# Optimization experiments

Hardware: AMD Instinct MI355X
Metric: run time of the kernel (lower is better)

The kernel has to match this reference:

```python
import jax, jax.numpy as jnp
import numpy as np

D_MODEL = 1024
N_HEADS = 16
HEAD_DIM = D_MODEL // N_HEADS
SEQ = 2048
BATCH = 2
ROPE_BASE = 10000.0


def _rope(x, start_pos):
    # x: [B, S, H, hd]; interleaved-pair RoPE (Llama view_as_complex convention)
    S, hd = x.shape[1], x.shape[3]
    inv_freq = 1.0 / (ROPE_BASE ** (jnp.arange(0, hd, 2, dtype=jnp.float32) / hd))
    pos = jnp.arange(start_pos, start_pos + S, dtype=jnp.float32)
    freqs = pos[:, None] * inv_freq[None, :]          # [S, hd/2]
    cos = jnp.cos(freqs)[None, :, None, :]            # [1, S, 1, hd/2]
    sin = jnp.sin(freqs)[None, :, None, :]
    x1 = x[..., 0::2]
    x2 = x[..., 1::2]
    r1 = x1 * cos - x2 * sin
    r2 = x1 * sin + x2 * cos
    return jnp.stack([r1, r2], axis=-1).reshape(x.shape)


def setup_inputs() -> dict:
    key = jax.random.key(0)
    ks = jax.random.split(key, 5)
    scale = 1.0 / np.sqrt(D_MODEL)
    x = jax.random.normal(ks[0], (BATCH, SEQ, D_MODEL), dtype=jnp.float32)
    Wq = jax.random.normal(ks[1], (D_MODEL, D_MODEL), dtype=jnp.float32) * scale
    Wk = jax.random.normal(ks[2], (D_MODEL, D_MODEL), dtype=jnp.float32) * scale
    Wv = jax.random.normal(ks[3], (D_MODEL, D_MODEL), dtype=jnp.float32) * scale
    Wo = jax.random.normal(ks[4], (D_MODEL, D_MODEL), dtype=jnp.float32) * scale
    # causal mask: True = masked (strictly upper triangular)
    mask = jnp.triu(jnp.ones((SEQ, SEQ), dtype=bool), k=1)[None, None, :, :]
    return {"x": x, "mask": mask, "Wq": Wq, "Wk": Wk, "Wv": Wv, "Wo": Wo}


def reference(x, mask, Wq, Wk, Wv, Wo):
    B, S, D = x.shape
    H, hd = N_HEADS, HEAD_DIM
    scale = 1.0 / np.sqrt(hd)
    start_pos = 0  # prefill, no kv_cache

    # torch nn.Linear(bias=False): y = x @ W.T
    q = jnp.einsum('bsd,ed->bse', x, Wq).reshape(B, S, H, hd)
    k = jnp.einsum('bsd,ed->bse', x, Wk).reshape(B, S, H, hd)
    v = jnp.einsum('bsd,ed->bse', x, Wv).reshape(B, S, H, hd)

    q = _rope(q, start_pos)
    k = _rope(k, start_pos)

    q = q.transpose(0, 2, 1, 3)  # [B, H, S, hd]
    k = k.transpose(0, 2, 1, 3)
    v = v.transpose(0, 2, 1, 3)
    new_kv_cache = (k, v)

    scores = jnp.einsum('bhqd,bhkd->bhqk', q, k) * scale   # [B,H,S,S]
    scores = jnp.where(mask, -jnp.inf, scores)
    attn = jax.nn.softmax(scores, axis=-1)                 # dropout is identity (eval)
    out = jnp.einsum('bhqk,bhkd->bhqd', attn, v)
    out = out.transpose(0, 2, 1, 3).reshape(B, S, D)
    out = jnp.einsum('bsd,ed->bse', out, Wo)
    return (out, new_kv_cache)
```

## Files before the change

kernel.cpp:

```cpp
#include <hip/hip_runtime.h>
#include <hip/hip_bf16.h>
#include <stdint.h>

#define D_MODEL 1024
#define SEQ     2048
#define BATCH   2
#define NH      16
#define HD      64
#define MROWS   (BATCH*SEQ)
#define XN      (MROWS*D_MODEL)
#define WN      (D_MODEL*D_MODEL)

typedef __attribute__((ext_vector_type(8))) __bf16 bf16x8;
typedef __attribute__((ext_vector_type(4))) __bf16 bf16x4;
typedef __attribute__((ext_vector_type(4))) float  floatx4;

#define MFMA(a,b,c) __builtin_amdgcn_mfma_f32_16x16x32_bf16((a),(b),(c),0,0,0)

__device__ __forceinline__ void g2l16(const void* g, void* l) {
    __builtin_amdgcn_global_load_lds(
        (const __attribute__((address_space(1))) void*)g,
        (__attribute__((address_space(3))) void*)l, 16, 0, 0);
}

__global__ __launch_bounds__(256) void cvt_kernel(
    const float* __restrict__ x,  const float* __restrict__ wq,
    const float* __restrict__ wk, const float* __restrict__ wv,
    const float* __restrict__ wo, __bf16* __restrict__ ws)
{
    const int y = blockIdx.y;
    const float* src;
    __bf16* dst;
    int n;
    if (y == 0) { src = x; dst = ws; n = XN; }
    else {
        n = WN;
        src = (y == 1) ? wq : (y == 2) ? wk : (y == 3) ? wv : wo;
        dst = ws + XN + (y - 1) * WN;
    }
    const int i = (blockIdx.x * 256 + threadIdx.x) * 4;
    if (i < n) {
        float4 f = *(const float4*)(src + i);
        bf16x4 o;
        o[0] = (__bf16)f.x; o[1] = (__bf16)f.y;
        o[2] = (__bf16)f.z; o[3] = (__bf16)f.w;
        *(bf16x4*)(dst + i) = o;
    }
}

__device__ __forceinline__ void gemm128_core(
    const __bf16* __restrict__ A, const __bf16* __restrict__ W,
    int m0, int n0, __bf16* ldsA, __bf16* ldsB, floatx4 acc[4][4])
{
    const int tid  = threadIdx.x;
    const int w    = tid >> 6;
    const int lane = tid & 63;
    const int quad = lane >> 4;
    const int ln   = lane & 15;
    const int wm   = (w >> 1) << 6;
    const int wn   = (w & 1) << 6;

    const int r0c = tid >> 2, ch = tid & 3;
    const __bf16* gA0 = A + (m0 + r0c) * D_MODEL + ch * 8;
    const __bf16* gA1 = gA0 + 64 * D_MODEL;
    const __bf16* gB0 = W + (n0 + r0c) * D_MODEL + ch * 8;
    const __bf16* gB1 = gB0 + 64 * D_MODEL;
    const int lofs = w * 512;

    g2l16(gA0, ldsA + lofs);
    g2l16(gA1, ldsA + 2048 + lofs);
    g2l16(gB0, ldsB + lofs);
    g2l16(gB1, ldsB + 2048 + lofs);
    __syncthreads();

    for (int k0 = 0; k0 < D_MODEL; k0 += 32) {
        const int cur = (k0 >> 5) & 1;
        const int nxt = cur ^ 1;
        if (k0 + 32 < D_MODEL) {
            g2l16(gA0 + k0 + 32, ldsA + nxt * 4096 + lofs);
            g2l16(gA1 + k0 + 32, ldsA + nxt * 4096 + 2048 + lofs);
            g2l16(gB0 + k0 + 32, ldsB + nxt * 4096 + lofs);
            g2l16(gB1 + k0 + 32, ldsB + nxt * 4096 + 2048 + lofs);
        }
        const __bf16* cA = ldsA + cur * 4096;
        const __bf16* cB = ldsB + cur * 4096;
        bf16x8 af[4], bfr[4];
        #pragma unroll
        for (int mt = 0; mt < 4; ++mt)
            af[mt] = *(const bf16x8*)(cA + (wm + mt * 16 + ln) * 32 + quad * 8);
        #pragma unroll
        for (int nt = 0; nt < 4; ++nt)
            bfr[nt] = *(const bf16x8*)(cB + (wn + nt * 16 + ln) * 32 + quad * 8);
        #pragma unroll
        for (int mt = 0; mt < 4; ++mt)
            #pragma unroll
            for (int nt = 0; nt < 4; ++nt)
                acc[mt][nt] = MFMA(af[mt], bfr[nt], acc[mt][nt]);
        __syncthreads();
    }
}

__global__ __launch_bounds__(256) void qkv_rope_kernel(
    const __bf16* __restrict__ x,  const __bf16* __restrict__ Wq,
    const __bf16* __restrict__ Wk, const __bf16* __restrict__ Wv,
    __bf16* __restrict__ q_ws, __bf16* __restrict__ k_bf,
    __bf16* __restrict__ vT_ws,
    float* __restrict__ k_out, float* __restrict__ v_out)
{
    const int id  = blockIdx.x;
    const int xcd = id & 7;
    const int sl  = id >> 3;
    const int mb  = (xcd & 3) * 8 + (sl & 7);
    const int yz  = (xcd >> 2) * 12 + (sl >> 3);
    const int nb  = yz & 7;
    const int which = yz >> 3;

    const __bf16* W = (which == 0) ? Wq : (which == 1) ? Wk : Wv;
    const int m0 = mb * 128;
    const int n0 = nb * 128;

    __shared__ __align__(16) __bf16 ldsA[2 * 128 * 32];
    __shared__ __align__(16) __bf16 ldsB[2 * 128 * 32];

    floatx4 acc[4][4] = {};
    gemm128_core(x, W, m0, n0, ldsA, ldsB, acc);

    const int lane = threadIdx.x & 63;
    const int w    = threadIdx.x >> 6;
    const int quad = lane >> 4;
    const int ln   = lane & 15;
    const int wm   = m0 + ((w >> 1) << 6);
    const int wn   = n0 + ((w & 1) << 6);

    #pragma unroll
    for (int nt = 0; nt < 4; ++nt) {
        const int e = wn + nt * 16 + ln;
        const int h = e >> 6;
        const int d = e & 63;
        const float invf = (which < 2)
            ? exp2f(-(float)(d & ~1) * 0.20762050593046014f) : 0.f;
        #pragma unroll
        for (int mt = 0; mt < 4; ++mt) {
            floatx4 c = acc[mt][nt];
            const int mbase = wm + mt * 16 + quad * 4;
            if (which < 2) {
                #pragma unroll
                for (int r = 0; r < 4; ++r) {
                    const int s = (mbase + r) & (SEQ - 1);
                    float self  = c[r];
                    float other = __shfl_xor(self, 1);
                    float sn, cs;
                    __sincosf((float)s * invf, &sn, &cs);
                    c[r] = (lane & 1) ? (other * sn + self * cs)
                                      : (self * cs - other * sn);
                }
            }
            const int b = mbase >> 11;
            const int s = mbase & (SEQ - 1);
            const int idx = ((b * NH + h) * SEQ + s) * HD + d;
            #pragma unroll
            for (int r = 0; r < 4; ++r) {
                if (which == 0) {
                    q_ws[idx + r * HD] = (__bf16)c[r];
                } else if (which == 1) {
                    k_out[idx + r * HD] = c[r];
                    k_bf[idx + r * HD]  = (__bf16)c[r];
                } else {
                    v_out[idx + r * HD] = c[r];
                }
            }
            if (which == 2) {
                bf16x4 pk;
                pk[0] = (__bf16)c[0]; pk[1] = (__bf16)c[1];
                pk[2] = (__bf16)c[2]; pk[3] = (__bf16)c[3];
                *(bf16x4*)(vT_ws + ((b * NH + h) * HD + d) * SEQ + s) = pk;
            }
        }
    }
}

__global__ __launch_bounds__(256, 4) void attn_kernel(
    const __bf16* __restrict__ q_ws, const __bf16* __restrict__ k_all,
    const __bf16* __restrict__ vT,   __bf16* __restrict__ attn_ws)
{
    const int id   = blockIdx.x;
    const int xcd  = id & 7;
    const int sl   = id >> 3;
    const int bh   = xcd * 4 + (sl & 3);
    const int qt   = 31 - (sl >> 2);
    const int w    = threadIdx.x >> 6;
    const int lane = threadIdx.x & 63;
    const int quad = lane >> 4;
    const int ln   = lane & 15;
    const int r0   = qt * 64 + w * 16;

    const __bf16* qb = q_ws + bh * SEQ * HD;
    const __bf16* kb = k_all + bh * SEQ * HD;
    const __bf16* vb = vT + bh * HD * SEQ;

    __shared__ __align__(16) __bf16 ldsK[2][64 * 64];
    __shared__ __align__(16) __bf16 ldsV[2][64 * 64];
    __shared__ __align__(16) __bf16 ldsp[4][16 * 64];
    __bf16* lp = &ldsp[w][0];

    const bf16x8 aq0 = *(const bf16x8*)(qb + (r0 + ln) * HD + quad * 8);
    const bf16x8 aq1 = *(const bf16x8*)(qb + (r0 + ln) * HD + 32 + quad * 8);

    const int nk = qt + 1;

    const int r8 = lane >> 3;
    const int cl = (lane & 7) ^ r8;
    const int rA = w * 16 + r8;
    const int rB = rA + 8;

    const int pc0 = ((quad    ) ^ (ln & 7)) << 3;
    const int pc1 = ((quad | 4) ^ (ln & 7)) << 3;

    auto stage = [&](int bsel, int j0) {
        g2l16(kb + (j0 + rA) * HD + cl * 8, &ldsK[bsel][(w * 16)     * 64]);
        g2l16(kb + (j0 + rB) * HD + cl * 8, &ldsK[bsel][(w * 16 + 8) * 64]);
        g2l16(vb + rA * SEQ + j0 + cl * 8,  &ldsV[bsel][(w * 16)     * 64]);
        g2l16(vb + rB * SEQ + j0 + cl * 8,  &ldsV[bsel][(w * 16 + 8) * 64]);
    };

    floatx4 acc[4] = {};
    float l_part[4] = {0.f, 0.f, 0.f, 0.f};

    stage(0, 0);
    __syncthreads();

    for (int tk = 0; tk < nk; ++tk) {
        const int buf = tk & 1;
        if (tk + 1 < nk) stage(buf ^ 1, (tk + 1) << 6);

        const __bf16* Kb = &ldsK[buf][0];
        const __bf16* Vb = &ldsV[buf][0];
        bf16x8 K[8], V[8];
        #pragma unroll
        for (int nt = 0; nt < 4; ++nt) {
            const int rowo = (nt * 16 + ln) * 64;
            K[nt * 2 + 0] = *(const bf16x8*)(Kb + rowo + pc0);
            K[nt * 2 + 1] = *(const bf16x8*)(Kb + rowo + pc1);
            V[nt * 2 + 0] = *(const bf16x8*)(Vb + rowo + pc0);
            V[nt * 2 + 1] = *(const bf16x8*)(Vb + rowo + pc1);
        }

        floatx4 s[4] = {};
        #pragma unroll
        for (int nt = 0; nt < 4; ++nt) {
            s[nt] = MFMA(aq0, K[nt * 2 + 0], s[nt]);
            s[nt] = MFMA(aq1, K[nt * 2 + 1], s[nt]);
        }

        if (tk == nk - 1) {
            const int j0 = tk << 6;
            #pragma unroll
            for (int nt = 0; nt < 4; ++nt) {
                const int col = j0 + nt * 16 + ln;
                #pragma unroll
                for (int r = 0; r < 4; ++r)
                    if (col > r0 + quad * 4 + r) s[nt][r] = -1e30f;
            }
        }

        floatx4 p[4];
        #pragma unroll
        for (int nt = 0; nt < 4; ++nt)
            #pragma unroll
            for (int r = 0; r < 4; ++r)
                p[nt][r] = __expf(fmaf(s[nt][r], 0.125f, -20.f));
        #pragma unroll
        for (int r = 0; r < 4; ++r)
            l_part[r] += (p[0][r] + p[1][r]) + (p[2][r] + p[3][r]);

        #pragma unroll
        for (int nt = 0; nt < 4; ++nt) {
            const int cchunk = nt * 2 + (ln >> 3);
            #pragma unroll
            for (int r = 0; r < 4; ++r) {
                const int row = quad * 4 + r;
                lp[row * 64 + ((cchunk ^ (row & 7)) << 3) + (ln & 7)] =
                    (__bf16)p[nt][r];
            }
        }
        const bf16x8 ap0 = *(const bf16x8*)(lp + ln * 64 + pc0);
        const bf16x8 ap1 = *(const bf16x8*)(lp + ln * 64 + pc1);

        #pragma unroll
        for (int nt = 0; nt < 4; ++nt) {
            acc[nt] = MFMA(ap0, V[nt * 2 + 0], acc[nt]);
            acc[nt] = MFMA(ap1, V[nt * 2 + 1], acc[nt]);
        }
        __syncthreads();
    }

    const int b = bh >> 4, h = bh & 15;
    #pragma unroll
    for (int r = 0; r < 4; ++r) {
        float l = l_part[r];
        l += __shfl_xor(l, 1);
        l += __shfl_xor(l, 2);
        l += __shfl_xor(l, 4);
        l += __shfl_xor(l, 8);
        const float inv = 1.f / fmaxf(l, 1e-37f);
        const int s = r0 + quad * 4 + r;
        #pragma unroll
        for (int nt = 0; nt < 4; ++nt) {
            attn_ws[(b * SEQ + s) * D_MODEL + h * HD + nt * 16 + ln] =
                (__bf16)(acc[nt][r] * inv);
        }
    }
}

__global__ __launch_bounds__(256) void out_proj_kernel(
    const __bf16* __restrict__ A, const __bf16* __restrict__ Wo,
    float* __restrict__ out)
{
    const int id  = blockIdx.x;
    const int xcd = id & 7;
    const int sl  = id >> 3;
    const int m0 = (xcd * 4 + (sl & 3)) * 128;
    const int n0 = (sl >> 2) * 128;

    __shared__ __align__(16) __bf16 ldsA[2 * 128 * 32];
    __shared__ __align__(16) __bf16 ldsB[2 * 128 * 32];

    floatx4 acc[4][4] = {};
    gemm128_core(A, Wo, m0, n0, ldsA, ldsB, acc);

    const int lane = threadIdx.x & 63;
    const int w    = threadIdx.x >> 6;
    const int quad = lane >> 4;
    const int ln   = lane & 15;
    const int wm   = m0 + ((w >> 1) << 6);
    const int wn   = n0 + ((w & 1) << 6);

    #pragma unroll
    for (int mt = 0; mt < 4; ++mt) {
        #pragma unroll
        for (int nt = 0; nt < 4; ++nt) {
            const floatx4 c = acc[mt][nt];
            const int e = wn + nt * 16 + ln;
            const int mbase = wm + mt * 16 + quad * 4;
            #pragma unroll
            for (int r = 0; r < 4; ++r)
                out[(mbase + r) * D_MODEL + e] = c[r];
        }
    }
}

extern "C" void kernel_launch(void* const* d_in, const int* in_sizes, int n_in,
                              void* d_out, int out_size, void* d_ws, size_t ws_size,
                              hipStream_t stream)
{
    (void)in_sizes; (void)n_in; (void)out_size; (void)ws_size;
    const float* x  = (const float*)d_in[0];
    const float* Wq = (const float*)d_in[2];
    const float* Wk = (const float*)d_in[3];
    const float* Wv = (const float*)d_in[4];
    const float* Wo = (const float*)d_in[5];

    float* out   = (float*)d_out;
    float* k_out = out + XN;
    float* v_out = k_out + XN;

    __bf16* ws      = (__bf16*)d_ws;
    __bf16* x_bf    = ws;
    __bf16* Wq_bf   = ws + XN;
    __bf16* Wk_bf   = Wq_bf + WN;
    __bf16* Wv_bf   = Wk_bf + WN;
    __bf16* Wo_bf   = Wv_bf + WN;
    __bf16* q_ws    = Wo_bf + WN;
    __bf16* k_bf    = q_ws + XN;
    __bf16* vT_ws   = k_bf + XN;
    __bf16* attn_ws = vT_ws + XN;

    dim3 gc(XN / 4 / 256, 5);
    cvt_kernel<<<gc, 256, 0, stream>>>(x, Wq, Wk, Wv, Wo, ws);

    qkv_rope_kernel<<<dim3(768), 256, 0, stream>>>(x_bf, Wq_bf, Wk_bf, Wv_bf,
                                                   q_ws, k_bf, vT_ws, k_out, v_out);

    attn_kernel<<<dim3(1024), 256, 0, stream>>>(q_ws, k_bf, vT_ws, attn_ws);

    out_proj_kernel<<<dim3(256), 256, 0, stream>>>(attn_ws, Wo_bf, out);
}
```

Before: 199.1 us.

## Make attention a persistent kernel with per-XCD atomic work queues

Replaces the one-block-per-tile attention grid with 768 persistent blocks. Each block reads its XCC id and pulls (head, query-tile) items from per-XCD atomic counters, ordering tiles as alternating short and long causal rows, and steals from other XCD queues once its own is empty. The goal is better load balance across the triangular causal work and less tail imbalance. The counters live in the output buffer, are zeroed by cvt_kernel, and are later overwritten by out_proj. Each item costs extra block-wide syncs for the atomic fetch.

```diff
diff --git a/kernel.cpp b/kernel.cpp
--- a/kernel.cpp
+++ b/kernel.cpp
@@ -26,8 +26,12 @@
 __global__ __launch_bounds__(256) void cvt_kernel(
     const float* __restrict__ x,  const float* __restrict__ wq,
     const float* __restrict__ wk, const float* __restrict__ wv,
-    const float* __restrict__ wo, __bf16* __restrict__ ws)
-{
+    const float* __restrict__ wo, __bf16* __restrict__ ws,
+    int* __restrict__ ctr)
+{
+    if (blockIdx.x == 0 && blockIdx.y == 0 && threadIdx.x < 8)
+        ctr[threadIdx.x] = 0;
+
     const int y = blockIdx.y;
     const float* src;
     __bf16* dst;
@@ -181,32 +185,19 @@
 
 __global__ __launch_bounds__(256, 4) void attn_kernel(
     const __bf16* __restrict__ q_ws, const __bf16* __restrict__ k_all,
-    const __bf16* __restrict__ vT,   __bf16* __restrict__ attn_ws)
-{
-    const int id   = blockIdx.x;
-    const int xcd  = id & 7;
-    const int sl   = id >> 3;
-    const int bh   = xcd * 4 + (sl & 3);
-    const int qt   = 31 - (sl >> 2);
+    const __bf16* __restrict__ vT,   __bf16* __restrict__ attn_ws,
+    int* __restrict__ ctr)
+{
     const int w    = threadIdx.x >> 6;
     const int lane = threadIdx.x & 63;
     const int quad = lane >> 4;
     const int ln   = lane & 15;
-    const int r0   = qt * 64 + w * 16;
-
-    const __bf16* qb = q_ws + bh * SEQ * HD;
-    const __bf16* kb = k_all + bh * SEQ * HD;
-    const __bf16* vb = vT + bh * HD * SEQ;
 
     __shared__ __align__(16) __bf16 ldsK[2][64 * 64];
     __shared__ __align__(16) __bf16 ldsV[2][64 * 64];
     __shared__ __align__(16) __bf16 ldsp[4][16 * 64];
+    __shared__ int sh_item;
     __bf16* lp = &ldsp[w][0];
-
-    const bf16x8 aq0 = *(const bf16x8*)(qb + (r0 + ln) * HD + quad * 8);
-    const bf16x8 aq1 = *(const bf16x8*)(qb + (r0 + ln) * HD + 32 + quad * 8);
-
-    const int nk = qt + 1;
 
     const int r8 = lane >> 3;
     const int cl = (lane & 7) ^ r8;
@@ -216,98 +207,125 @@
     const int pc0 = ((quad    ) ^ (ln & 7)) << 3;
     const int pc1 = ((quad | 4) ^ (ln & 7)) << 3;
 
-    auto stage = [&](int bsel, int j0) {
-        g2l16(kb + (j0 + rA) * HD + cl * 8, &ldsK[bsel][(w * 16)     * 64]);
-        g2l16(kb + (j0 + rB) * HD + cl * 8, &ldsK[bsel][(w * 16 + 8) * 64]);
-        g2l16(vb + rA * SEQ + j0 + cl * 8,  &ldsV[bsel][(w * 16)     * 64]);
-        g2l16(vb + rB * SEQ + j0 + cl * 8,  &ldsV[bsel][(w * 16 + 8) * 64]);
-    };
-
-    floatx4 acc[4] = {};
-    float l_part[4] = {0.f, 0.f, 0.f, 0.f};
-
-    stage(0, 0);
-    __syncthreads();
-
-    for (int tk = 0; tk < nk; ++tk) {
-        const int buf = tk & 1;
-        if (tk + 1 < nk) stage(buf ^ 1, (tk + 1) << 6);
-
-        const __bf16* Kb = &ldsK[buf][0];
-        const __bf16* Vb = &ldsV[buf][0];
-        bf16x8 K[8], V[8];
-        #pragma unroll
-        for (int nt = 0; nt < 4; ++nt) {
-            const int rowo = (nt * 16 + ln) * 64;
-            K[nt * 2 + 0] = *(const bf16x8*)(Kb + rowo + pc0);
-            K[nt * 2 + 1] = *(const bf16x8*)(Kb + rowo + pc1);
-            V[nt * 2 + 0] = *(const bf16x8*)(Vb + rowo + pc0);
-            V[nt * 2 + 1] = *(const bf16x8*)(Vb + rowo + pc1);
-        }
-
-        floatx4 s[4] = {};
-        #pragma unroll
-        for (int nt = 0; nt < 4; ++nt) {
-            s[nt] = MFMA(aq0, K[nt * 2 + 0], s[nt]);
-            s[nt] = MFMA(aq1, K[nt * 2 + 1], s[nt]);
-        }
-
-        if (tk == nk - 1) {
-            const int j0 = tk << 6;
-            #pragma unroll
-            for (int nt = 0; nt < 4; ++nt) {
-                const int col = j0 + nt * 16 + ln;
+    unsigned xcc;
+    asm volatile("s_getreg_b32 %0, hwreg(HW_REG_XCC_ID)" : "=s"(xcc));
+
+    for (int qo = 0; qo < 8; ++qo) {
+        const int q = (int)((xcc + qo) & 7);
+        for (;;) {
+            if (threadIdx.x == 0) sh_item = atomicAdd(ctr + q, 1);
+            __syncthreads();
+            const int it = sh_item;
+            __syncthreads();
+            if (it >= 128) break;
+
+            const int u  = it & 31;
+            const int bh = q * 4 + (it >> 5);
+            const int qt = (u & 1) ? (31 - (u >> 1)) : (u >> 1);
+            const int r0 = qt * 64 + w * 16;
+            const int nk = qt + 1;
+
+            const __bf16* qb = q_ws + bh * SEQ * HD;
+            const __bf16* kb = k_all + bh * SEQ * HD;
+            const __bf16* vb = vT + bh * HD * SEQ;
+
+            const bf16x8 aq0 = *(const bf16x8*)(qb + (r0 + ln) * HD + quad * 8);
+            const bf16x8 aq1 = *(const bf16x8*)(qb + (r0 + ln) * HD + 32 + quad * 8);
+
+            auto stage = [&](int bsel, int j0) {
+                g2l16(kb + (j0 + rA) * HD + cl * 8, &ldsK[bsel][(w * 16)     * 64]);
+                g2l16(kb + (j0 + rB) * HD + cl * 8, &ldsK[bsel][(w * 16 + 8) * 64]);
+                g2l16(vb + rA * SEQ + j0 + cl * 8,  &ldsV[bsel][(w * 16)     * 64]);
+                g2l16(vb + rB * SEQ + j0 + cl * 8,  &ldsV[bsel][(w * 16 + 8) * 64]);
+            };
+
+            floatx4 acc[4] = {};
+            float l_part[4] = {0.f, 0.f, 0.f, 0.f};
+
+            stage(0, 0);
+            __syncthreads();
+
+            for (int tk = 0; tk < nk; ++tk) {
+                const int buf = tk & 1;
+                if (tk + 1 < nk) stage(buf ^ 1, (tk + 1) << 6);
+
+                const __bf16* Kb = &ldsK[buf][0];
+                const __bf16* Vb = &ldsV[buf][0];
+                bf16x8 K[8], V[8];
+                #pragma unroll
+                for (int nt = 0; nt < 4; ++nt) {
+                    const int rowo = (nt * 16 + ln) * 64;
+                    K[nt * 2 + 0] = *(const bf16x8*)(Kb + rowo + pc0);
+                    K[nt * 2 + 1] = *(const bf16x8*)(Kb + rowo + pc1);
+                    V[nt * 2 + 0] = *(const bf16x8*)(Vb + rowo + pc0);
+                    V[nt * 2 + 1] = *(const bf16x8*)(Vb + rowo + pc1);
+                }
+
+                floatx4 s[4] = {};
+                #pragma unroll
+                for (int nt = 0; nt < 4; ++nt) {
+                    s[nt] = MFMA(aq0, K[nt * 2 + 0], s[nt]);
+                    s[nt] = MFMA(aq1, K[nt * 2 + 1], s[nt]);
+                }
+
+                if (tk == nk - 1) {
+                    const int j0 = tk << 6;
+                    #pragma unroll
+                    for (int nt = 0; nt < 4; ++nt) {
+                        const int col = j0 + nt * 16 + ln;
+                        #pragma unroll
+                        for (int r = 0; r < 4; ++r)
+                            if (col > r0 + quad * 4 + r) s[nt][r] = -1e30f;
+                    }
+                }
+
+                floatx4 p[4];
+                #pragma unroll
+                for (int nt = 0; nt < 4; ++nt)
+                    #pragma unroll
+                    for (int r = 0; r < 4; ++r)
+                        p[nt][r] = __expf(fmaf(s[nt][r], 0.125f, -20.f));
                 #pragma unroll
                 for (int r = 0; r < 4; ++r)
-                    if (col > r0 + quad * 4 + r) s[nt][r] = -1e30f;
+                    l_part[r] += (p[0][r] + p[1][r]) + (p[2][r] + p[3][r]);
+
+                #pragma unroll
+                for (int nt = 0; nt < 4; ++nt) {
+                    const int cchunk = nt * 2 + (ln >> 3);
+                    #pragma unroll
+                    for (int r = 0; r < 4; ++r) {
+                        const int row = quad * 4 + r;
+                        lp[row * 64 + ((cchunk ^ (row & 7)) << 3) + (ln & 7)] =
+                            (__bf16)p[nt][r];
+                    }
+                }
+                const bf16x8 ap0 = *(const bf16x8*)(lp + ln * 64 + pc0);
+                const bf16x8 ap1 = *(const bf16x8*)(lp + ln * 64 + pc1);
+
+                #pragma unroll
+                for (int nt = 0; nt < 4; ++nt) {
+                    acc[nt] = MFMA(ap0, V[nt * 2 + 0], acc[nt]);
+                    acc[nt] = MFMA(ap1, V[nt * 2 + 1], acc[nt]);
+                }
+                __syncthreads();
             }
-        }
-
-        floatx4 p[4];
-        #pragma unroll
-        for (int nt = 0; nt < 4; ++nt)
-            #pragma unroll
-            for (int r = 0; r < 4; ++r)
-                p[nt][r] = __expf(fmaf(s[nt][r], 0.125f, -20.f));
-        #pragma unroll
-        for (int r = 0; r < 4; ++r)
-            l_part[r] += (p[0][r] + p[1][r]) + (p[2][r] + p[3][r]);
-
-        #pragma unroll
-        for (int nt = 0; nt < 4; ++nt) {
-            const int cchunk = nt * 2 + (ln >> 3);
+
+            const int b = bh >> 4, h = bh & 15;
             #pragma unroll
             for (int r = 0; r < 4; ++r) {
-                const int row = quad * 4 + r;
-                lp[row * 64 + ((cchunk ^ (row & 7)) << 3) + (ln & 7)] =
-                    (__bf16)p[nt][r];
+                float l = l_part[r];
+                l += __shfl_xor(l, 1);
+                l += __shfl_xor(l, 2);
+                l += __shfl_xor(l, 4);
+                l += __shfl_xor(l, 8);
+                const float inv = 1.f / fmaxf(l, 1e-37f);
+                const int s = r0 + quad * 4 + r;
+                #pragma unroll
+                for (int nt = 0; nt < 4; ++nt) {
+                    attn_ws[(b * SEQ + s) * D_MODEL + h * HD + nt * 16 + ln] =
+                        (__bf16)(acc[nt][r] * inv);
+                }
             }
-        }
-        const bf16x8 ap0 = *(const bf16x8*)(lp + ln * 64 + pc0);
-        const bf16x8 ap1 = *(const bf16x8*)(lp + ln * 64 + pc1);
-
-        #pragma unroll
-        for (int nt = 0; nt < 4; ++nt) {
-            acc[nt] = MFMA(ap0, V[nt * 2 + 0], acc[nt]);
-            acc[nt] = MFMA(ap1, V[nt * 2 + 1], acc[nt]);
-        }
-        __syncthreads();
-    }
-
-    const int b = bh >> 4, h = bh & 15;
-    #pragma unroll
-    for (int r = 0; r < 4; ++r) {
-        float l = l_part[r];
-        l += __shfl_xor(l, 1);
-        l += __shfl_xor(l, 2);
-        l += __shfl_xor(l, 4);
-        l += __shfl_xor(l, 8);
-        const float inv = 1.f / fmaxf(l, 1e-37f);
-        const int s = r0 + quad * 4 + r;
-        #pragma unroll
-        for (int nt = 0; nt < 4; ++nt) {
-            attn_ws[(b * SEQ + s) * D_MODEL + h * HD + nt * 16 + ln] =
-                (__bf16)(acc[nt][r] * inv);
         }
     }
 }
@@ -364,6 +382,8 @@
     float* k_out = out + XN;
     float* v_out = k_out + XN;
 
+    int* ctr = (int*)out;
+
     __bf16* ws      = (__bf16*)d_ws;
     __bf16* x_bf    = ws;
     __bf16* Wq_bf   = ws + XN;
@@ -376,12 +396,12 @@
     __bf16* attn_ws = vT_ws + XN;
 
     dim3 gc(XN / 4 / 256, 5);
-    cvt_kernel<<<gc, 256, 0, stream>>>(x, Wq, Wk, Wv, Wo, ws);
+    cvt_kernel<<<gc, 256, 0, stream>>>(x, Wq, Wk, Wv, Wo, ws, ctr);
 
     qkv_rope_kernel<<<dim3(768), 256, 0, stream>>>(x_bf, Wq_bf, Wk_bf, Wv_bf,
                                                    q_ws, k_bf, vT_ws, k_out, v_out);
 
-    attn_kernel<<<dim3(1024), 256, 0, stream>>>(q_ws, k_bf, vT_ws, attn_ws);
+    attn_kernel<<<dim3(768), 256, 0, stream>>>(q_ws, k_bf, vT_ws, attn_ws, ctr);
 
     out_proj_kernel<<<dim3(256), 256, 0, stream>>>(attn_ws, Wo_bf, out);
 }
```

Result: slower. 262.1 us (+31.6%).
